# Kernel optimization log

Hardware: AMD Instinct MI355X
Metric: run time of the kernel (lower is better)

Reference implementation:

```python
import jax, jax.numpy as jnp
import numpy as np
import math

B, S, KV, D, H = 4, 512, 4096, 1024, 16
HD = D // H  # head_dim = 64


def setup_inputs() -> dict:
    key = jax.random.key(0)
    ks = jax.random.split(key, 12)
    scale = 0.02
    return {
        "x": jax.random.normal(ks[0], (B, S, D), dtype=jnp.float32),
        "xa": jax.random.normal(ks[1], (B, KV, D), dtype=jnp.float32),
        "Wq": jax.random.normal(ks[2], (D, D), dtype=jnp.float32) * scale,
        "bq": jax.random.normal(ks[3], (D,), dtype=jnp.float32) * scale,
        "Wk": jax.random.normal(ks[4], (D, D), dtype=jnp.float32) * scale,  # key has no bias
        "Wv": jax.random.normal(ks[5], (D, D), dtype=jnp.float32) * scale,
        "bv": jax.random.normal(ks[6], (D,), dtype=jnp.float32) * scale,
        "Wo": jax.random.normal(ks[7], (D, D), dtype=jnp.float32) * scale,
        "bo": jax.random.normal(ks[8], (D,), dtype=jnp.float32) * scale,
        "cache_k": jnp.zeros((B, H, KV, HD), dtype=jnp.float32),
        "cache_v": jnp.zeros((B, H, KV, HD), dtype=jnp.float32),
    }


def reference(x, xa, Wq, bq, Wk, Wv, bv, Wo, bo, cache_k, cache_v):
    bsz, seq_len, _ = x.shape
    kv_len = xa.shape[1]
    # projections (torch nn.Linear convention: y = x @ W^T + b)
    q = (x @ Wq.T + bq).reshape(bsz, seq_len, H, HD).transpose(0, 2, 1, 3)   # [B,H,S,HD]
    k = (xa @ Wk.T).reshape(bsz, kv_len, H, HD).transpose(0, 2, 1, 3)        # [B,H,KV,HD]
    v = (xa @ Wv.T + bv).reshape(bsz, kv_len, H, HD).transpose(0, 2, 1, 3)   # [B,H,KV,HD]
    # prefill path: scatter k/v into positions [0, kv_len) of the cache
    updated_k = cache_k.at[:, :, :kv_len, :].set(k)
    updated_v = cache_v.at[:, :, :kv_len, :].set(v)
    # attention over full cache, fp32 softmax as in the original
    scores = jnp.einsum('bhqd,bhkd->bhqk', q, updated_k) / math.sqrt(HD)
    probs = jax.nn.softmax(scores.astype(jnp.float32), axis=-1).astype(q.dtype)
    attn = jnp.einsum('bhqk,bhkd->bhqd', probs, updated_v)                   # [B,H,S,HD]
    attn = attn.transpose(0, 2, 1, 3).reshape(bsz, seq_len, H * HD)
    out = attn @ Wo.T + bo
    return out, updated_k, updated_v
```

## Files before the change

### kernel.cpp

```cpp
#include <hip/hip_runtime.h>
#include <hip/hip_bf16.h>

using u16 = unsigned short;
typedef __bf16 bf16x8 __attribute__((ext_vector_type(8)));
typedef float f32x4 __attribute__((ext_vector_type(4)));

#define SB 4
#define SS 512
#define SKV 4096
#define SD 1024
#define SH 16
#define SHD 64
#define NSPLIT 4
#define NROWS 32768
#define QSCALE 0.18033688011112042f
#define DEFER_THR 6.0f

__device__ inline u16 f2bf(float f){
  __hip_bfloat16 h = __float2bfloat16(f);
  return __builtin_bit_cast(u16, h);
}
__device__ inline float bf2f(u16 u){
  return __builtin_bit_cast(float, (unsigned)u << 16);
}

__device__ inline bf16x8 ld_frag_g(const u16* p){
  uint4 v = *reinterpret_cast<const uint4*>(p);
  return __builtin_bit_cast(bf16x8, v);
}

__device__ inline bf16x8 ld_frag_lds(const char* base, int ob){
  uint4 v = *reinterpret_cast<const uint4*>(base + ob);
  return __builtin_bit_cast(bf16x8, v);
}

__device__ inline unsigned pack_bf_trunc(float a, float b){
  return __builtin_amdgcn_perm(__builtin_bit_cast(unsigned, b),
                               __builtin_bit_cast(unsigned, a), 0x07060302u);
}

__global__ __launch_bounds__(256) void cast_kernel(const float* __restrict__ src,
                                                   u16* __restrict__ dst, int n4){
  int i = blockIdx.x * 256 + threadIdx.x;
  if (i < n4){
    float4 f = reinterpret_cast<const float4*>(src)[i];
    ushort4 u;
    u.x = f2bf(f.x); u.y = f2bf(f.y); u.z = f2bf(f.z); u.w = f2bf(f.w);
    reinterpret_cast<ushort4*>(dst)[i] = u;
  }
}

__global__ __launch_bounds__(256) void cast_w4(const float* __restrict__ s0,
                                               const float* __restrict__ s1,
                                               const float* __restrict__ s2,
                                               const float* __restrict__ s3,
                                               u16* __restrict__ dst){
  int which = blockIdx.x >> 10;
  int j = (blockIdx.x & 1023) * 256 + threadIdx.x;
  const float* s = which == 0 ? s0 : which == 1 ? s1 : which == 2 ? s2 : s3;
  float4 f = reinterpret_cast<const float4*>(s)[j];
  ushort4 u;
  u.x = f2bf(f.x); u.y = f2bf(f.y); u.z = f2bf(f.z); u.w = f2bf(f.w);
  reinterpret_cast<ushort4*>(dst + (long)which * 1048576L)[j] = u;
}

enum { MODE_Q = 0, MODE_K = 1, MODE_V = 2, MODE_OUT = 3 };

template<int MODE, int SWZ>
__global__ __launch_bounds__(256) void gemm_bt(const u16* __restrict__ A,
                                               const u16* __restrict__ W,
                                               const float* __restrict__ bias,
                                               float* __restrict__ outF,
                                               u16* __restrict__ outB)
{
  __shared__ u16 As[128*64];
  __shared__ u16 Bs[128*64];
  const int tid  = threadIdx.x;
  const int lane = tid & 63;
  const int wm   = ((tid >> 6) >> 1) * 64;
  const int wn   = ((tid >> 6) & 1) * 64;
  long rowBase, colBase;
  if (SWZ){
    int lin = blockIdx.x;
    int xcd = lin & 7, j = lin >> 3;
    int row = xcd * 16 + (j >> 3);
    int col = j & 7;
    rowBase = (long)row * 128;
    colBase = (long)col * 128;
  } else {
    rowBase = (long)blockIdx.x * 128;
    colBase = (long)blockIdx.y * 128;
  }

  f32x4 acc[4][4];
#pragma unroll
  for (int i = 0; i < 4; i++)
#pragma unroll
    for (int j = 0; j < 4; j++)
      acc[i][j] = (f32x4){0.f, 0.f, 0.f, 0.f};

  for (int kt = 0; kt < 16; ++kt){
    __syncthreads();
#pragma unroll
    for (int i = 0; i < 4; i++){
      int u = tid + i * 256;
      int r = u >> 3, c = u & 7;
      uint4 va = *reinterpret_cast<const uint4*>(A + (rowBase + r) * 1024 + kt * 64 + c * 8);
      uint4 vw = *reinterpret_cast<const uint4*>(W + (colBase + r) * 1024 + kt * 64 + c * 8);
      int ob = (r * 128 + c * 16) ^ ((r & 7) << 4);
      *reinterpret_cast<uint4*>(reinterpret_cast<char*>(As) + ob) = va;
      *reinterpret_cast<uint4*>(reinterpret_cast<char*>(Bs) + ob) = vw;
    }
    __syncthreads();
#pragma unroll
    for (int kk = 0; kk < 2; kk++){
      bf16x8 af[4], bfr[4];
#pragma unroll
      for (int mi = 0; mi < 4; mi++){
        int row = wm + mi * 16 + (lane & 15);
        int ob = (row * 128 + kk * 64 + (lane >> 4) * 16) ^ ((row & 7) << 4);
        af[mi] = ld_frag_lds(reinterpret_cast<const char*>(As), ob);
      }
#pragma unroll
      for (int ni = 0; ni < 4; ni++){
        int row = wn + ni * 16 + (lane & 15);
        int ob = (row * 128 + kk * 64 + (lane >> 4) * 16) ^ ((row & 7) << 4);
        bfr[ni] = ld_frag_lds(reinterpret_cast<const char*>(Bs), ob);
      }
#pragma unroll
      for (int mi = 0; mi < 4; mi++)
#pragma unroll
        for (int ni = 0; ni < 4; ni++)
          acc[mi][ni] = __builtin_amdgcn_mfma_f32_16x16x32_bf16(af[mi], bfr[ni], acc[mi][ni], 0, 0, 0);
    }
  }

#pragma unroll
  for (int mi = 0; mi < 4; mi++){
#pragma unroll
    for (int ni = 0; ni < 4; ni++){
      long gn = colBase + wn + ni * 16 + (lane & 15);
      float bb = 0.f;
      if (MODE == MODE_Q || MODE == MODE_V || MODE == MODE_OUT) bb = bias[gn];
      if (MODE == MODE_V){
        long gmBase = rowBase + wm + mi * 16 + ((lane >> 4) << 2);
        long b = gmBase >> 12, kv = gmBase & 4095;
        long h = gn >> 6, hd = gn & 63;
        long fidx = ((b * SH + h) * SKV + kv) * SHD + hd;
        ushort4 pk;
        float v0 = acc[mi][ni][0] + bb; outF[fidx          ] = v0; pk.x = f2bf(v0);
        float v1 = acc[mi][ni][1] + bb; outF[fidx +     SHD] = v1; pk.y = f2bf(v1);
        float v2 = acc[mi][ni][2] + bb; outF[fidx + 2 * SHD] = v2; pk.z = f2bf(v2);
        float v3 = acc[mi][ni][3] + bb; outF[fidx + 3 * SHD] = v3; pk.w = f2bf(v3);
        *reinterpret_cast<ushort4*>(outB + ((b * SH + h) * SHD + hd) * SKV + kv) = pk;
      } else {
#pragma unroll
        for (int r = 0; r < 4; r++){
          long gm = rowBase + wm + mi * 16 + ((lane >> 4) << 2) + r;
          float val = acc[mi][ni][r] + bb;
          if (MODE == MODE_OUT){
            outF[gm * 1024 + gn] = val;
          } else if (MODE == MODE_Q){
            long b = gm >> 9, s = gm & 511;
            long h = gn >> 6, hd = gn & 63;
            outB[((b * SH + h) * SS + s) * SHD + hd] = f2bf(val * QSCALE);
          } else {
            long b = gm >> 12, kv = gm & 4095;
            long h = gn >> 6, hd = gn & 63;
            long idx = ((b * SH + h) * SKV + kv) * SHD + hd;
            outF[idx] = val;
            outB[idx] = f2bf(val);
          }
        }
      }
    }
  }
}

__global__ __launch_bounds__(512) void attn_partial(const u16* __restrict__ qb,
                                                    const u16* __restrict__ kb,
                                                    const u16* __restrict__ vTb,
                                                    u16* __restrict__ opartB,
                                                    float* __restrict__ ml){
  __shared__ u16 Klds[64 * 64];
  __shared__ u16 Vlds[64 * 64];
  __shared__ u16 PT[8][16 * 72];
  const int tid  = threadIdx.x;
  const int lane = tid & 63;
  const int wid  = tid >> 6;
  const int c    = lane & 15;
  const int hi   = lane >> 4;
  const long bh  = blockIdx.x;
  const int  qt  = blockIdx.y;
  const int  split = blockIdx.z;

  const u16* qp = qb + (bh * SS + qt * 128 + wid * 16 + c) * SHD + hi * 8;
  const bf16x8 bq0 = ld_frag_g(qp);
  const bf16x8 bq1 = ld_frag_g(qp + 32);

  f32x4 acc[4];
#pragma unroll
  for (int i = 0; i < 4; i++) acc[i] = (f32x4){0.f, 0.f, 0.f, 0.f};
  float mrun = -INFINITY;
  f32x4 lrunv = (f32x4){0.f, 0.f, 0.f, 0.f};

  const u16* kbase = kb  + bh * SKV * SHD;
  const u16* vbase = vTb + bh * SHD * SKV;
  u16* pt = &PT[wid][0];
  char* kch = reinterpret_cast<char*>(Klds);
  char* vch = reinterpret_cast<char*>(Vlds);

  for (int kt = split * 16; kt < split * 16 + 16; ++kt){
    __syncthreads();
    {
      int u = tid;
      int r = u >> 3, cc = u & 7;
      uint4 kv4 = *reinterpret_cast<const uint4*>(kbase + (kt * 64 + r) * SHD + cc * 8);
      uint4 vv4 = *reinterpret_cast<const uint4*>(vbase + (long)r * SKV + kt * 64 + cc * 8);
      int ob = (r * 128 + cc * 16) ^ ((r & 7) << 4);
      *reinterpret_cast<uint4*>(kch + ob) = kv4;
      *reinterpret_cast<uint4*>(vch + ob) = vv4;
    }
    __syncthreads();

    f32x4 sT[4];
#pragma unroll
    for (int ni = 0; ni < 4; ni++){
      int krow = ni * 16 + c;
      int swz = (krow & 7) << 4;
      int a0 = (krow * 128 + hi * 16) ^ swz;
      int a1 = (krow * 128 + 64 + hi * 16) ^ swz;
      f32x4 z = (f32x4){0.f, 0.f, 0.f, 0.f};
      sT[ni] = __builtin_amdgcn_mfma_f32_16x16x32_bf16(ld_frag_lds(kch, a0), bq0, z, 0, 0, 0);
      sT[ni] = __builtin_amdgcn_mfma_f32_16x16x32_bf16(ld_frag_lds(kch, a1), bq1, sT[ni], 0, 0, 0);
    }
    f32x4 mv = __builtin_elementwise_max(__builtin_elementwise_max(sT[0], sT[1]),
                                         __builtin_elementwise_max(sT[2], sT[3]));
    float t = fmaxf(fmaxf(mv[0], mv[1]), fmaxf(mv[2], mv[3]));
    if (!__all(t <= mrun + DEFER_THR)){
      float tr = fmaxf(t, __shfl_xor(t, 16));
      tr = fmaxf(tr, __shfl_xor(tr, 32));
      float mn = fmaxf(mrun, tr);
      float al = exp2f(mrun - mn);
      lrunv *= al;
#pragma unroll
      for (int ni = 0; ni < 4; ni++) acc[ni] *= al;
      mrun = mn;
    }
#pragma unroll
    for (int ni = 0; ni < 4; ni++){
      f32x4 p;
      p[0] = exp2f(sT[ni][0] - mrun); p[1] = exp2f(sT[ni][1] - mrun);
      p[2] = exp2f(sT[ni][2] - mrun); p[3] = exp2f(sT[ni][3] - mrun);
      lrunv += p;
      unsigned lo = pack_bf_trunc(p[0], p[1]);
      unsigned hp = pack_bf_trunc(p[2], p[3]);
      uint2 w; w.x = lo; w.y = hp;
      *reinterpret_cast<uint2*>(pt + c * 72 + ni * 16 + hi * 4) = w;
    }
#pragma unroll
    for (int m = 0; m < 2; m++){
      bf16x8 pfrag = __builtin_bit_cast(bf16x8,
          *reinterpret_cast<const uint4*>(pt + c * 72 + m * 32 + hi * 8));
#pragma unroll
      for (int ni = 0; ni < 4; ni++){
        int vrow = ni * 16 + c;
        int av = (vrow * 128 + m * 64 + hi * 16) ^ ((vrow & 7) << 4);
        acc[ni] = __builtin_amdgcn_mfma_f32_16x16x32_bf16(ld_frag_lds(vch, av), pfrag, acc[ni], 0, 0, 0);
      }
    }
  }

  float l = (lrunv[0] + lrunv[1]) + (lrunv[2] + lrunv[3]);
  l += __shfl_xor(l, 16);
  l += __shfl_xor(l, 32);
  const long row = bh * SS + (long)qt * 128 + wid * 16 + c;
  u16* ob = opartB + ((long)split * NROWS + row) * SHD;
#pragma unroll
  for (int ni = 0; ni < 4; ni++){
    ushort4 pk;
    pk.x = f2bf(acc[ni][0]); pk.y = f2bf(acc[ni][1]);
    pk.z = f2bf(acc[ni][2]); pk.w = f2bf(acc[ni][3]);
    *reinterpret_cast<ushort4*>(ob + ni * 16 + hi * 4) = pk;
  }
  if (hi == 0){
    ml[(long)split * NROWS + row] = mrun;
    ml[(long)NSPLIT * NROWS + (long)split * NROWS + row] = l;
  }
}

__global__ __launch_bounds__(256) void attn_combine(const u16* __restrict__ opartB,
                                                    const float* __restrict__ ml,
                                                    u16* __restrict__ attnb){
  long idx4 = (long)blockIdx.x * 256 + threadIdx.x;
  long row = idx4 >> 4;
  int  c   = (int)(idx4 & 15);
  float m0 = ml[row], m1 = ml[NROWS + row], m2 = ml[2L*NROWS + row], m3 = ml[3L*NROWS + row];
  float M = fmaxf(fmaxf(m0, m1), fmaxf(m2, m3));
  float w0 = exp2f(m0 - M), w1 = exp2f(m1 - M), w2 = exp2f(m2 - M), w3 = exp2f(m3 - M);
  const float* lb = ml + (long)NSPLIT * NROWS;
  float L = w0*lb[row] + w1*lb[NROWS+row] + w2*lb[2L*NROWS+row] + w3*lb[3L*NROWS+row];
  float inv = 1.f / L;
  const ushort4* op = reinterpret_cast<const ushort4*>(opartB);
  ushort4 v0 = op[(0L*NROWS + row) * 16 + c];
  ushort4 v1 = op[(1L*NROWS + row) * 16 + c];
  ushort4 v2 = op[(2L*NROWS + row) * 16 + c];
  ushort4 v3 = op[(3L*NROWS + row) * 16 + c];
  float4 val;
  val.x = (w0*bf2f(v0.x) + w1*bf2f(v1.x) + w2*bf2f(v2.x) + w3*bf2f(v3.x)) * inv;
  val.y = (w0*bf2f(v0.y) + w1*bf2f(v1.y) + w2*bf2f(v2.y) + w3*bf2f(v3.y)) * inv;
  val.z = (w0*bf2f(v0.z) + w1*bf2f(v1.z) + w2*bf2f(v2.z) + w3*bf2f(v3.z)) * inv;
  val.w = (w0*bf2f(v0.w) + w1*bf2f(v1.w) + w2*bf2f(v2.w) + w3*bf2f(v3.w)) * inv;
  long bh = row >> 9, s = row & 511;
  long b = bh >> 4, h = bh & 15;
  ushort4 u;
  u.x = f2bf(val.x); u.y = f2bf(val.y); u.z = f2bf(val.z); u.w = f2bf(val.w);
  reinterpret_cast<ushort4*>(attnb)[((b * SS + s) * SD + h * SHD) / 4 + c] = u;
}

extern "C" void kernel_launch(void* const* d_in, const int* in_sizes, int n_in,
                              void* d_out, int out_size, void* d_ws, size_t ws_size,
                              hipStream_t stream)
{
  const float* x  = (const float*)d_in[0];
  const float* xa = (const float*)d_in[1];
  const float* Wq = (const float*)d_in[2];
  const float* bq = (const float*)d_in[3];
  const float* Wk = (const float*)d_in[4];
  const float* Wv = (const float*)d_in[5];
  const float* bv = (const float*)d_in[6];
  const float* Wo = (const float*)d_in[7];
  const float* bo = (const float*)d_in[8];

  float* outO = (float*)d_out;
  float* outK = outO + (long)SB * SS * SD;
  float* outV = outK + (long)SB * SH * SKV * SHD;

  u16* ws   = (u16*)d_ws;
  u16* xb   = ws;
  u16* xab  = xb   + 2097152L;
  u16* Wqb  = xab  + 16777216L;
  u16* Wkb  = Wqb  + 1048576L;
  u16* Wvb  = Wkb  + 1048576L;
  u16* Wob  = Wvb  + 1048576L;
  u16* qbuf = Wob  + 1048576L;
  u16* kbuf = qbuf + 2097152L;
  u16* vTbuf= kbuf + 16777216L;
  u16* mlb  = vTbuf+ 16777216L;

  u16*   attnb  = xb;
  u16*   opartB = xab;
  float* ml     = (float*)mlb;

  cast_kernel<<<2048, 256, 0, stream>>>(x,  xb,  524288);
  cast_kernel<<<16384, 256, 0, stream>>>(xa, xab, 4194304);
  cast_w4    <<<4096, 256, 0, stream>>>(Wq, Wk, Wv, Wo, Wqb);

  gemm_bt<MODE_Q, 0>  <<<dim3(16, 8), 256, 0, stream>>>(xb,  Wqb, bq, nullptr, qbuf);
  gemm_bt<MODE_K, 1>  <<<1024,        256, 0, stream>>>(xab, Wkb, nullptr, outK, kbuf);
  gemm_bt<MODE_V, 1>  <<<1024,        256, 0, stream>>>(xab, Wvb, bv, outV, vTbuf);
  attn_partial        <<<dim3(64, 4, NSPLIT), 512, 0, stream>>>(qbuf, kbuf, vTbuf, opartB, ml);
  attn_combine        <<<2048, 256, 0, stream>>>(opartB, ml, attnb);
  gemm_bt<MODE_OUT, 0><<<dim3(16, 8), 256, 0, stream>>>(attnb, Wob, bo, outO, nullptr);
}
```

Measured before the change: 258.1 us.

## Double-buffer LDS tiles with register prefetch in GEMM and attention kernels

Both the projection GEMM and the attention partial kernel now prefetch the next K-tile from global memory into registers while computing on the current LDS buffer. The prefetched data is then stored into a second LDS buffer, which cuts one barrier per iteration. This hides global load latency behind MFMA work. In exchange it doubles LDS usage and raises register pressure, which may reduce occupancy.

```diff
diff --git a/kernel.cpp b/kernel.cpp
--- a/kernel.cpp
+++ b/kernel.cpp
@@ -73,8 +73,8 @@
                                                float* __restrict__ outF,
                                                u16* __restrict__ outB)
 {
-  __shared__ u16 As[128*64];
-  __shared__ u16 Bs[128*64];
+  __shared__ u16 As[2][128*64];
+  __shared__ u16 Bs[2][128*64];
   const int tid  = threadIdx.x;
   const int lane = tid & 63;
   const int wm   = ((tid >> 6) >> 1) * 64;
@@ -99,19 +99,38 @@
     for (int j = 0; j < 4; j++)
       acc[i][j] = (f32x4){0.f, 0.f, 0.f, 0.f};
 
+  uint4 va[4], vw[4];
+#pragma unroll
+  for (int i = 0; i < 4; i++){
+    int u = tid + i * 256;
+    int r = u >> 3, c = u & 7;
+    va[i] = *reinterpret_cast<const uint4*>(A + (rowBase + r) * 1024 + c * 8);
+    vw[i] = *reinterpret_cast<const uint4*>(W + (colBase + r) * 1024 + c * 8);
+  }
+#pragma unroll
+  for (int i = 0; i < 4; i++){
+    int u = tid + i * 256;
+    int r = u >> 3, c = u & 7;
+    int ob = (r * 128 + c * 16) ^ ((r & 7) << 4);
+    *reinterpret_cast<uint4*>(reinterpret_cast<char*>(As[0]) + ob) = va[i];
+    *reinterpret_cast<uint4*>(reinterpret_cast<char*>(Bs[0]) + ob) = vw[i];
+  }
+  __syncthreads();
+
+  int cur = 0;
   for (int kt = 0; kt < 16; ++kt){
-    __syncthreads();
-#pragma unroll
-    for (int i = 0; i < 4; i++){
-      int u = tid + i * 256;
-      int r = u >> 3, c = u & 7;
-      uint4 va = *reinterpret_cast<const uint4*>(A + (rowBase + r) * 1024 + kt * 64 + c * 8);
-      uint4 vw = *reinterpret_cast<const uint4*>(W + (colBase + r) * 1024 + kt * 64 + c * 8);
-      int ob = (r * 128 + c * 16) ^ ((r & 7) << 4);
-      *reinterpret_cast<uint4*>(reinterpret_cast<char*>(As) + ob) = va;
-      *reinterpret_cast<uint4*>(reinterpret_cast<char*>(Bs) + ob) = vw;
-    }
-    __syncthreads();
+    uint4 va2[4], vw2[4];
+    if (kt < 15){
+#pragma unroll
+      for (int i = 0; i < 4; i++){
+        int u = tid + i * 256;
+        int r = u >> 3, c = u & 7;
+        va2[i] = *reinterpret_cast<const uint4*>(A + (rowBase + r) * 1024 + (kt + 1) * 64 + c * 8);
+        vw2[i] = *reinterpret_cast<const uint4*>(W + (colBase + r) * 1024 + (kt + 1) * 64 + c * 8);
+      }
+    }
+    const char* ach = reinterpret_cast<const char*>(As[cur]);
+    const char* bch = reinterpret_cast<const char*>(Bs[cur]);
 #pragma unroll
     for (int kk = 0; kk < 2; kk++){
       bf16x8 af[4], bfr[4];
@@ -119,13 +138,13 @@
       for (int mi = 0; mi < 4; mi++){
         int row = wm + mi * 16 + (lane & 15);
         int ob = (row * 128 + kk * 64 + (lane >> 4) * 16) ^ ((row & 7) << 4);
-        af[mi] = ld_frag_lds(reinterpret_cast<const char*>(As), ob);
+        af[mi] = ld_frag_lds(ach, ob);
       }
 #pragma unroll
       for (int ni = 0; ni < 4; ni++){
         int row = wn + ni * 16 + (lane & 15);
         int ob = (row * 128 + kk * 64 + (lane >> 4) * 16) ^ ((row & 7) << 4);
-        bfr[ni] = ld_frag_lds(reinterpret_cast<const char*>(Bs), ob);
+        bfr[ni] = ld_frag_lds(bch, ob);
       }
 #pragma unroll
       for (int mi = 0; mi < 4; mi++)
@@ -133,6 +152,18 @@
         for (int ni = 0; ni < 4; ni++)
           acc[mi][ni] = __builtin_amdgcn_mfma_f32_16x16x32_bf16(af[mi], bfr[ni], acc[mi][ni], 0, 0, 0);
     }
+    if (kt < 15){
+#pragma unroll
+      for (int i = 0; i < 4; i++){
+        int u = tid + i * 256;
+        int r = u >> 3, c = u & 7;
+        int ob = (r * 128 + c * 16) ^ ((r & 7) << 4);
+        *reinterpret_cast<uint4*>(reinterpret_cast<char*>(As[cur ^ 1]) + ob) = va2[i];
+        *reinterpret_cast<uint4*>(reinterpret_cast<char*>(Bs[cur ^ 1]) + ob) = vw2[i];
+      }
+      __syncthreads();
+    }
+    cur ^= 1;
   }
 
 #pragma unroll
@@ -182,8 +213,8 @@
                                                     const u16* __restrict__ vTb,
                                                     u16* __restrict__ opartB,
                                                     float* __restrict__ ml){
-  __shared__ u16 Klds[64 * 64];
-  __shared__ u16 Vlds[64 * 64];
+  __shared__ u16 Klds[2][64 * 64];
+  __shared__ u16 Vlds[2][64 * 64];
   __shared__ u16 PT[8][16 * 72];
   const int tid  = threadIdx.x;
   const int lane = tid & 63;
@@ -207,21 +238,29 @@
   const u16* kbase = kb  + bh * SKV * SHD;
   const u16* vbase = vTb + bh * SHD * SKV;
   u16* pt = &PT[wid][0];
-  char* kch = reinterpret_cast<char*>(Klds);
-  char* vch = reinterpret_cast<char*>(Vlds);
-
-  for (int kt = split * 16; kt < split * 16 + 16; ++kt){
-    __syncthreads();
-    {
-      int u = tid;
-      int r = u >> 3, cc = u & 7;
-      uint4 kv4 = *reinterpret_cast<const uint4*>(kbase + (kt * 64 + r) * SHD + cc * 8);
-      uint4 vv4 = *reinterpret_cast<const uint4*>(vbase + (long)r * SKV + kt * 64 + cc * 8);
-      int ob = (r * 128 + cc * 16) ^ ((r & 7) << 4);
-      *reinterpret_cast<uint4*>(kch + ob) = kv4;
-      *reinterpret_cast<uint4*>(vch + ob) = vv4;
-    }
-    __syncthreads();
+  const int sr  = tid >> 3;
+  const int scc = tid & 7;
+  const int sob = (sr * 128 + scc * 16) ^ ((sr & 7) << 4);
+  const int t0 = split * 16;
+
+  {
+    uint4 kv4 = *reinterpret_cast<const uint4*>(kbase + (t0 * 64 + sr) * SHD + scc * 8);
+    uint4 vv4 = *reinterpret_cast<const uint4*>(vbase + (long)sr * SKV + t0 * 64 + scc * 8);
+    *reinterpret_cast<uint4*>(reinterpret_cast<char*>(Klds[0]) + sob) = kv4;
+    *reinterpret_cast<uint4*>(reinterpret_cast<char*>(Vlds[0]) + sob) = vv4;
+  }
+  __syncthreads();
+
+  int cur = 0;
+  for (int kt = t0; kt < t0 + 16; ++kt){
+    const bool hn = kt + 1 < t0 + 16;
+    uint4 kn, vn;
+    if (hn){
+      kn = *reinterpret_cast<const uint4*>(kbase + ((kt + 1) * 64 + sr) * SHD + scc * 8);
+      vn = *reinterpret_cast<const uint4*>(vbase + (long)sr * SKV + (kt + 1) * 64 + scc * 8);
+    }
+    const char* kch = reinterpret_cast<const char*>(Klds[cur]);
+    const char* vch = reinterpret_cast<const char*>(Vlds[cur]);
 
     f32x4 sT[4];
 #pragma unroll
@@ -269,6 +308,12 @@
         acc[ni] = __builtin_amdgcn_mfma_f32_16x16x32_bf16(ld_frag_lds(vch, av), pfrag, acc[ni], 0, 0, 0);
       }
     }
+    if (hn){
+      *reinterpret_cast<uint4*>(reinterpret_cast<char*>(Klds[cur ^ 1]) + sob) = kn;
+      *reinterpret_cast<uint4*>(reinterpret_cast<char*>(Vlds[cur ^ 1]) + sob) = vn;
+      __syncthreads();
+    }
+    cur ^= 1;
   }
 
   float l = (lrunv[0] + lrunv[1]) + (lrunv[2] + lrunv[3]);
```

New measurement: 254.4 us. Within noise of the previous version (-1.5%).
